# Kernel optimization log

Measured on AMD Instinct MI355X. Metric: run time of the kernel, lower is better.

## Reference

```python
import jax, jax.numpy as jnp
import numpy as np
import math

EPS = 1e-7
N, M, K, D_IN, D_OUT = 8192, 32, 8, 64, 64
KP_EXTENT = 0.66

# ---- Lorentz manifold (curvature k = 1) helpers ----

def l_inner(x, y):
    # Lorentzian inner product, keepdim on last axis
    return -x[..., :1] * y[..., :1] + jnp.sum(x[..., 1:] * y[..., 1:], axis=-1, keepdims=True)

def l_dist(x, y):
    alpha = jnp.clip(-l_inner(x, y), 1.0 + EPS, None)
    return jnp.arccosh(alpha)[..., 0]

def expmap0(u):
    # u: tangent at origin, time component ignored-by-construction (zero)
    sp = u[..., 1:]
    un = jnp.sqrt(jnp.clip(jnp.sum(sp * sp, axis=-1, keepdims=True), 1e-14, None))
    return jnp.concatenate([jnp.cosh(un), jnp.sinh(un) * sp / un], axis=-1)

def expmap(x, u):
    un = jnp.sqrt(jnp.clip(l_inner(u, u), 1e-14, None))
    return jnp.cosh(un) * x + jnp.sinh(un) * u / un

def logmap(x, y):
    alpha = jnp.clip(-l_inner(x, y), 1.0 + EPS, None)
    d = jnp.arccosh(alpha)
    nom = y - alpha * x
    den = jnp.sqrt(jnp.clip(alpha * alpha - 1.0, 1e-14, None))
    return d * nom / den

def ptransp(x, y, v):
    # parallel transport of v from x to y
    return v + l_inner(y, v) / (1.0 - l_inner(x, y)) * (x + y)

def norm_midpoint(ave):
    den = jnp.sqrt(jnp.clip(jnp.abs(l_inner(ave, ave)), 1e-8, None))
    return ave / den


def setup_inputs() -> dict:
    key = jax.random.key(0)
    k1, k2, k3, k4, k5, k6 = jax.random.split(key, 6)
    # points on the hyperboloid: time = sqrt(1 + ||space||^2)
    sp = jax.random.normal(k1, (N, D_IN - 1), dtype=jnp.float32) * 0.5
    t = jnp.sqrt(1.0 + jnp.sum(sp * sp, axis=-1, keepdims=True))
    x = jnp.concatenate([t, sp], axis=-1)
    nei = jax.random.randint(k2, (N, M), 0, N, dtype=jnp.int32)
    nei_mask = jax.random.randint(k3, (N, M), 0, 2, dtype=jnp.int32)
    # kernel points: tangent vectors at origin (time comp 0), first point = center
    kp_sp = jax.random.normal(k4, (K, D_IN - 1), dtype=jnp.float32)
    kp_sp = kp_sp / jnp.linalg.norm(kp_sp, axis=-1, keepdims=True)
    radii = jax.random.uniform(k5, (K, 1), dtype=jnp.float32) * KP_EXTENT
    kp_sp = kp_sp * radii
    kp_sp = kp_sp.at[0].set(0.0)
    kernel_points = jnp.concatenate([jnp.zeros((K, 1), jnp.float32), kp_sp], axis=-1)
    # K LorentzLinear params
    stdv = 1.0 / math.sqrt(D_OUT)
    W = jax.random.uniform(k6, (K, D_OUT, D_IN), dtype=jnp.float32, minval=-stdv, maxval=stdv)
    W = W.at[:, :, 0].set(0.0)  # reset_parameters zeros first input column
    b = jnp.zeros((K, D_OUT), dtype=jnp.float32)
    scale = jnp.full((K,), math.log(10.0), dtype=jnp.float32)
    return {"x": x, "nei": nei, "nei_mask": nei_mask, "W": W, "b": b,
            "scale": scale, "kernel_points": kernel_points}


def reference(x, nei, nei_mask, W, b, scale, kernel_points):
    n, d = x.shape
    x_nei = x[nei]                      # [n, m, d] gather
    xr = x[:, None, :]                  # [n, 1, d]
    og_row = jnp.zeros((d,), x.dtype).at[0].set(1.0)
    # transport_x: map each neighborhood to the origin's tangent frame
    v = logmap(xr, x_nei)
    x0_nei = expmap0(ptransp(xr, og_row[None, None, :], v))   # [n, m, d]
    # kernel positions at the origin (transp=True => base point is origin)
    tmp = expmap(og_row[None, :], ptransp(og_row[None, :], og_row[None, :], kernel_points[1:]))
    x_kernel = jnp.concatenate([tmp, og_row[None, :]], axis=0)  # [K, d]
    # geodesic distances neighbor <-> kernel point: [n, K, m]
    dis = l_dist(x0_nei[:, None, :, :], x_kernel[None, :, None, :])
    dis = dis * nei_mask[:, None, :].astype(x.dtype)
    # K LorentzLinear transforms (vectorized over K): [n, K, m, d_out]
    h = jnp.einsum('nmd,kod->nkmo', x0_nei, W) + b[None, :, None, :]
    time = jax.nn.sigmoid(h[..., :1]) * jnp.exp(scale)[None, :, None, None] + 1.0001
    nar = h[..., 1:]
    s = (time * time - 1.0) / jnp.clip(jnp.sum(nar * nar, axis=-1, keepdims=True), 1e-8, None)
    xt = jnp.concatenate([time, nar * jnp.sqrt(s)], axis=-1)
    # weighted Lorentz midpoint over kernel points, per neighbor: [n, m, d_out]
    per_nei = norm_midpoint(jnp.einsum('nkm,nkmo->nmo', dis, xt))
    # unweighted Lorentz midpoint over neighbors: [n, d_out]
    return norm_midpoint(per_nei.mean(axis=1))
```

## Files before the change

### kernel.cpp

```cpp
#include <hip/hip_runtime.h>
#include <hip/hip_bf16.h>

#define N_NODES 8192
#define M_NEI   32
#define K_PTS   8
#define D       64
#define EPS_    1e-7f

typedef float f4v __attribute__((ext_vector_type(4)));
typedef short s8v __attribute__((ext_vector_type(8)));

__device__ __forceinline__ ushort f2bf(float f) {
  __hip_bfloat16 h = __float2bfloat16(f);
  return *reinterpret_cast<ushort*>(&h);
}
__device__ __forceinline__ float bf2f(ushort u) {
  __hip_bfloat16 h;
  *reinterpret_cast<ushort*>(&h) = u;
  return __bfloat162float(h);
}
__device__ __forceinline__ float frcp(float x)  { return __builtin_amdgcn_rcpf(x); }
__device__ __forceinline__ float frsq(float x)  { return __builtin_amdgcn_rsqf(x); }
__device__ __forceinline__ float fsqrt(float x) { return __builtin_amdgcn_sqrtf(x); }
__device__ __forceinline__ float facosh(float a) {
  float den = fsqrt(fmaxf(a * a - 1.f, 1e-14f));
  return __logf(a + den);
}

template<int CTRL>
__device__ __forceinline__ float dppadd(float v) {
  int t = __builtin_amdgcn_update_dpp(0, __float_as_int(v), CTRL, 0xf, 0xf, true);
  return v + __int_as_float(t);
}
template<int CTRL>
__device__ __forceinline__ float dppmov(float v) {
  return __int_as_float(__builtin_amdgcn_update_dpp(0, __float_as_int(v), CTRL, 0xf, 0xf, true));
}
__device__ __forceinline__ float swz_xor4(float v) {
  return __int_as_float(__builtin_amdgcn_ds_swizzle(__float_as_int(v), 0x101F));
}
__device__ __forceinline__ float sum8(float v) {
  v = dppadd<0xB1>(v);
  v = dppadd<0x4E>(v);
  v = dppadd<0x141>(v);
  return v;
}
__device__ __forceinline__ float sum16(float v) {
  v = dppadd<0x121>(v);
  v = dppadd<0x122>(v);
  v = dppadd<0x124>(v);
  v = dppadd<0x128>(v);
  return v;
}

__global__ void prep_xk(const float* __restrict__ kp, const float* __restrict__ scale,
                        float* __restrict__ xk) {
  int d = threadIdx.x;
  for (int kk = 0; kk < K_PTS - 1; ++kk) {
    float v = kp[(kk + 1) * D + d];
    float p = (d == 0) ? 0.f : v * v;
    #pragma unroll
    for (int s = 1; s < 64; s <<= 1) p += __shfl_xor(p, s);
    float un = sqrtf(fmaxf(p, 1e-14f));
    float sh = sinhf(un) / un;
    xk[kk * D + d] = (d == 0) ? coshf(un) : sh * v;
  }
  xk[(K_PTS - 1) * D + d] = (d == 0) ? 1.f : 0.f;
  if (d < K_PTS) xk[K_PTS * D + d] = expf(scale[d]);
}

__global__ void prep_wb(const float* __restrict__ W, ushort* __restrict__ WF) {
  int idx = blockIdx.x * 256 + threadIdx.x;
  int k    = idx >> 9;
  int ct   = (idx >> 7) & 3;
  int ks   = (idx >> 6) & 1;
  int lane = idx & 63;
  int o  = ct * 16 + (lane & 15);
  int db = (lane >> 4) * 8 + ks * 32;
  const float* wrow = W + (k * 64 + o) * 64 + db;
  s8v hi, lo;
  #pragma unroll
  for (int j = 0; j < 8; ++j) {
    float w = wrow[j];
    ushort h = f2bf(w);
    hi[j] = (short)h;
    lo[j] = (short)f2bf(w - bf2f(h));
  }
  int f = (k * 4 + ct) * 2 + ks;
  *(s8v*)(WF + (size_t)(f * 2 + 0) * 512 + lane * 8) = hi;
  *(s8v*)(WF + (size_t)(f * 2 + 1) * 512 + lane * 8) = lo;
}

__launch_bounds__(256, 4)
__global__ void kpa_main(const float* __restrict__ x, const int* __restrict__ nei,
                         const int* __restrict__ mask, const ushort* __restrict__ WF,
                         const float* __restrict__ b, const float* __restrict__ scale,
                         const float* __restrict__ xk, float* __restrict__ out) {
  __shared__ __align__(16) float  xr_s[D];
  __shared__ __align__(16) float  xk_s[K_PTS * D];
  __shared__ __align__(16) ushort Ah_lds[M_NEI * D];
  __shared__ __align__(16) ushort Al_lds[M_NEI * D];
  __shared__ float dis_s[K_PTS * 33];
  __shared__ __align__(8)  float  hss[K_PTS * M_NEI * 2];
  __shared__ __align__(16) float  red_h[2][16 * 68];
  __shared__ __align__(16) float  redp2[2][64];

  const int n  = blockIdx.x;
  const int t  = threadIdx.x;
  const int w4 = t >> 6;
  const int l  = t & 63;
  const int cl = l & 15;
  const int gr = l >> 4;
  const int wm = w4 & 1;
  const int wk = w4 >> 1;

  if (t < D) xr_s[t] = x[n * D + t];
  xk_s[t] = xk[t]; xk_s[t + 256] = xk[t + 256];
  __syncthreads();

  {
    const int m  = t >> 3;
    const int l8 = t & 7;
    const int d0 = l8 * 8;
    const int ni = nei[n * M_NEI + m];
    float y[8], xr[8];
    float y0 = x[ni * D];
    {
      float4 ya = *(const float4*)(x + ni * D + d0);
      float4 yb = *(const float4*)(x + ni * D + d0 + 4);
      y[0]=ya.x; y[1]=ya.y; y[2]=ya.z; y[3]=ya.w;
      y[4]=yb.x; y[5]=yb.y; y[6]=yb.z; y[7]=yb.w;
      float4 ra = *(const float4*)(xr_s + d0);
      float4 rb = *(const float4*)(xr_s + d0 + 4);
      xr[0]=ra.x; xr[1]=ra.y; xr[2]=ra.z; xr[3]=ra.w;
      xr[4]=rb.x; xr[5]=rb.y; xr[6]=rb.z; xr[7]=rb.w;
    }
    const float xr0 = xr_s[0];
    float p = 0.f;
    #pragma unroll
    for (int j = 0; j < 8; ++j) p += xr[j] * y[j];
    if (l8 == 0) p -= 2.f * xr[0] * y[0];
    p = sum8(p);
    float alpha = fmaxf(-p, 1.f + EPS_);
    float den = fsqrt(fmaxf(alpha * alpha - 1.f, 1e-14f));
    float dd  = __logf(alpha + den);
    float f   = dd * frcp(den);
    float v[8];
    #pragma unroll
    for (int j = 0; j < 8; ++j) v[j] = f * (y[j] - alpha * xr[j]);
    float v0 = f * (y0 - alpha * xr0);
    float c  = -v0 * frcp(1.f + xr0);
    float wv[8];
    float q = 0.f;
    #pragma unroll
    for (int j = 0; j < 8; ++j) { wv[j] = v[j] + c * xr[j]; q += wv[j] * wv[j]; }
    if (l8 == 0) q -= wv[0] * wv[0];
    q = sum8(q);
    float un = fsqrt(fmaxf(q, 1e-14f));
    float e  = __expf(un);
    float ei = frcp(e);
    float sh = (0.5f * (e - ei)) * frcp(un);
    float x0v[8];
    #pragma unroll
    for (int j = 0; j < 8; ++j) x0v[j] = sh * wv[j];
    if (l8 == 0) x0v[0] = 0.5f * (e + ei);
    {
      s8v hi, lo;
      #pragma unroll
      for (int j = 0; j < 8; ++j) {
        uint u = __float_as_uint(x0v[j]);
        hi[j] = (short)(ushort)(u >> 16);
        float lof = x0v[j] - __uint_as_float(u & 0xffff0000u);
        uint ul = __float_as_uint(lof);
        lo[j] = (short)(ushort)((ul + 0x7fffu + ((ul >> 16) & 1u)) >> 16);
      }
      int byte = m * 128 + d0 * 2;
      int swz  = byte ^ ((m & 7) << 4);
      *(s8v*)((char*)Ah_lds + swz) = hi;
      *(s8v*)((char*)Al_lds + swz) = lo;
    }
    float msk = (float)mask[n * M_NEI + m];
    if (l8 == 0) x0v[0] = -x0v[0];
    float pk[8];
    #pragma unroll
    for (int kk = 0; kk < K_PTS; ++kk) {
      const float* xkp = xk_s + kk * D + d0;
      float pp = 0.f;
      #pragma unroll
      for (int j = 0; j < 8; ++j) pp += x0v[j] * xkp[j];
      pk[kk] = pp;
    }
    const bool hi4 = (l8 & 4);
    float s1[4];
    #pragma unroll
    for (int j = 0; j < 4; ++j) {
      float give = hi4 ? pk[j] : pk[j + 4];
      float keep = hi4 ? pk[j + 4] : pk[j];
      s1[j] = keep + swz_xor4(give);
    }
    const bool hi2 = (l8 & 2);
    float s2[2];
    #pragma unroll
    for (int j = 0; j < 2; ++j) {
      float give = hi2 ? s1[j] : s1[j + 2];
      float keep = hi2 ? s1[j + 2] : s1[j];
      s2[j] = keep + dppmov<0x4E>(give);
    }
    const bool hi1 = (l8 & 1);
    float give = hi1 ? s2[0] : s2[1];
    float keep = hi1 ? s2[1] : s2[0];
    float mypp = keep + dppmov<0xB1>(give);
    float al_ = fmaxf(-mypp, 1.f + EPS_);
    dis_s[l8 * 33 + m] = facosh(al_) * msk;
  }
  __syncthreads();

  const int row = wm * 16 + cl;
  s8v ah[2], alo[2];
  #pragma unroll
  for (int ks = 0; ks < 2; ++ks) {
    int byte = row * 128 + (gr * 8 + ks * 32) * 2;
    int swz  = byte ^ ((row & 7) << 4);
    ah[ks]  = *(const s8v*)((const char*)Ah_lds + swz);
    alo[ks] = *(const s8v*)((const char*)Al_lds + swz);
  }

  f4v acc[4][4];
  #pragma unroll
  for (int kq = 0; kq < 4; ++kq) {
    const int k = wk * 4 + kq;
    #pragma unroll
    for (int ct = 0; ct < 4; ++ct) {
      float bv = b[k * 64 + ct * 16 + cl];
      f4v a = (f4v){bv, bv, bv, bv};
      #pragma unroll
      for (int ks = 0; ks < 2; ++ks) {
        int fi = (k * 4 + ct) * 2 + ks;
        s8v bh = *(const s8v*)(WF + (size_t)(fi * 2 + 0) * 512 + l * 8);
        s8v bl = *(const s8v*)(WF + (size_t)(fi * 2 + 1) * 512 + l * 8);
        a = __builtin_amdgcn_mfma_f32_16x16x32_bf16(ah[ks],  bh, a, 0, 0, 0);
        a = __builtin_amdgcn_mfma_f32_16x16x32_bf16(ah[ks],  bl, a, 0, 0, 0);
        a = __builtin_amdgcn_mfma_f32_16x16x32_bf16(alo[ks], bh, a, 0, 0, 0);
      }
      acc[kq][ct] = a;
    }
    #pragma unroll
    for (int r = 0; r < 4; ++r) {
      float ss = acc[kq][0][r]*acc[kq][0][r] + acc[kq][1][r]*acc[kq][1][r]
               + acc[kq][2][r]*acc[kq][2][r] + acc[kq][3][r]*acc[kq][3][r];
      ss = sum16(ss);
      if (cl == 0) {
        const int m = wm * 16 + gr * 4 + r;
        float2* hp = (float2*)&hss[(k * M_NEI + m) * 2];
        *hp = make_float2(acc[kq][0][r], ss);
      }
    }
  }
  __syncthreads();

  {
    const int k = t >> 5;
    const int m = t & 31;
    float2 hp = *(const float2*)&hss[(k * M_NEI + m) * 2];
    float h0 = hp.x, ss = hp.y;
    float nar2 = fmaxf(ss - h0 * h0, 1e-8f);
    float es   = xk[K_PTS * D + k];
    float time = es * frcp(1.f + __expf(-h0)) + 1.0001f;
    float sq   = fsqrt(time * time - 1.f) * frsq(nar2);
    float dm   = dis_s[k * 33 + m];
    *(float2*)&hss[(k * M_NEI + m) * 2] = make_float2(dm * sq, dm * time);
  }
  __syncthreads();

  float yacc[4][4];
  #pragma unroll
  for (int r = 0; r < 4; ++r)
    #pragma unroll
    for (int ct = 0; ct < 4; ++ct) yacc[r][ct] = 0.f;

  #pragma unroll
  for (int kq = 0; kq < 4; ++kq) {
    const int k = wk * 4 + kq;
    #pragma unroll
    for (int r = 0; r < 4; ++r) {
      const int m = wm * 16 + gr * 4 + r;
      float2 dd = *(const float2*)&hss[(k * M_NEI + m) * 2];
      yacc[r][0] += (cl == 0) ? dd.y : dd.x * acc[kq][0][r];
      yacc[r][1] += dd.x * acc[kq][1][r];
      yacc[r][2] += dd.x * acc[kq][2][r];
      yacc[r][3] += dd.x * acc[kq][3][r];
    }
  }

  if (wk == 1) {
    #pragma unroll
    for (int r = 0; r < 4; ++r) {
      const int ml = gr * 4 + r;
      float* rw = &red_h[wm][ml * 68];
      rw[cl]      = yacc[r][0];
      rw[16 + cl] = yacc[r][1];
      rw[32 + cl] = yacc[r][2];
      rw[48 + cl] = yacc[r][3];
    }
  }
  __syncthreads();

  if (wk == 0) {
    float s[4] = {0.f, 0.f, 0.f, 0.f};
    #pragma unroll
    for (int r = 0; r < 4; ++r) {
      const int ml = gr * 4 + r;
      const float* rw = &red_h[wm][ml * 68];
      float v0_ = yacc[r][0] + rw[cl];
      float v1_ = yacc[r][1] + rw[16 + cl];
      float v2_ = yacc[r][2] + rw[32 + cl];
      float v3_ = yacc[r][3] + rw[48 + cl];
      float ip = v0_*v0_ + v1_*v1_ + v2_*v2_ + v3_*v3_;
      if (cl == 0) ip -= 2.f * v0_ * v0_;
      ip = sum16(ip);
      float rin = frsq(fmaxf(fabsf(ip), 1e-8f));
      s[0] += v0_ * rin; s[1] += v1_ * rin;
      s[2] += v2_ * rin; s[3] += v3_ * rin;
    }
    #pragma unroll
    for (int j = 0; j < 4; ++j) {
      float z = s[j];
      z += __shfl_xor(z, 16); z += __shfl_xor(z, 32);
      s[j] = z;
    }
    if (gr == 0) {
      #pragma unroll
      for (int j = 0; j < 4; ++j) redp2[wm][j * 16 + cl] = s[j];
    }
  }
  __syncthreads();

  if (t < 16) {
    float mv[4]; float ip = 0.f;
    #pragma unroll
    for (int j = 0; j < 4; ++j) {
      mv[j] = (redp2[0][j * 16 + t] + redp2[1][j * 16 + t]) * (1.f / 32.f);
      ip += mv[j] * mv[j];
    }
    if (t == 0) ip -= 2.f * mv[0] * mv[0];
    ip = sum16(ip);
    float rin = frsq(fmaxf(fabsf(ip), 1e-8f));
    #pragma unroll
    for (int j = 0; j < 4; ++j) out[n * D + j * 16 + t] = mv[j] * rin;
  }
}

extern "C" void kernel_launch(void* const* d_in, const int* in_sizes, int n_in,
                              void* d_out, int out_size, void* d_ws, size_t ws_size,
                              hipStream_t stream) {
  const float* x     = (const float*)d_in[0];
  const int*   nei   = (const int*)d_in[1];
  const int*   mask  = (const int*)d_in[2];
  const float* W     = (const float*)d_in[3];
  const float* b     = (const float*)d_in[4];
  const float* scale = (const float*)d_in[5];
  const float* kp    = (const float*)d_in[6];
  float* out = (float*)d_out;

  ushort* WF = (ushort*)d_ws;
  float*  xk = (float*)(WF + 65536);

  prep_wb<<<16, 256, 0, stream>>>(W, WF);
  prep_xk<<<1, 64, 0, stream>>>(kp, scale, xk);
  kpa_main<<<N_NODES, 256, 0, stream>>>(x, nei, mask, WF, b, scale, xk, out);
}
```

Baseline: 103.2 us.

## Remove block barriers by wave-local hss handoff and split final reduction across waves

The per-block x row is now read straight from global memory instead of being staged in LDS, which removes the first barrier. The h-to-weight stage is remapped so each wave processes only the hss entries it wrote, which removes two __syncthreads. The cross-wave reduction is split so all four waves each normalise half the rows, and the final midpoint runs on 64 lanes instead of 16. The goal is to cut barrier stalls and idle waves in a short, latency-bound kernel. Correctness now depends on LDS ordering within a wave, with no block barrier between the hss write and read.

```diff
diff --git a/kernel.cpp b/kernel.cpp
--- a/kernel.cpp
+++ b/kernel.cpp
@@ -96,14 +96,13 @@
                          const int* __restrict__ mask, const ushort* __restrict__ WF,
                          const float* __restrict__ b, const float* __restrict__ scale,
                          const float* __restrict__ xk, float* __restrict__ out) {
-  __shared__ __align__(16) float  xr_s[D];
-  __shared__ __align__(16) float  xk_s[K_PTS * D];
+  __shared__ __align__(16) float  xk_s[K_PTS * D + 8];
   __shared__ __align__(16) ushort Ah_lds[M_NEI * D];
   __shared__ __align__(16) ushort Al_lds[M_NEI * D];
   __shared__ float dis_s[K_PTS * 33];
   __shared__ __align__(8)  float  hss[K_PTS * M_NEI * 2];
-  __shared__ __align__(16) float  red_h[2][16 * 68];
-  __shared__ __align__(16) float  redp2[2][64];
+  __shared__ __align__(16) float  red_e[2][2][8 * 68];
+  __shared__ __align__(16) float  redp3[4][64];
 
   const int n  = blockIdx.x;
   const int t  = threadIdx.x;
@@ -114,15 +113,15 @@
   const int wm = w4 & 1;
   const int wk = w4 >> 1;
 
-  if (t < D) xr_s[t] = x[n * D + t];
   xk_s[t] = xk[t]; xk_s[t + 256] = xk[t + 256];
-  __syncthreads();
-
+  if (t < 8) xk_s[512 + t] = xk[512 + t];
+
+  const int mP  = t >> 3;
+  const int l8  = t & 7;
+  float x0v[8];
   {
-    const int m  = t >> 3;
-    const int l8 = t & 7;
     const int d0 = l8 * 8;
-    const int ni = nei[n * M_NEI + m];
+    const int ni = nei[n * M_NEI + mP];
     float y[8], xr[8];
     float y0 = x[ni * D];
     {
@@ -130,12 +129,12 @@
       float4 yb = *(const float4*)(x + ni * D + d0 + 4);
       y[0]=ya.x; y[1]=ya.y; y[2]=ya.z; y[3]=ya.w;
       y[4]=yb.x; y[5]=yb.y; y[6]=yb.z; y[7]=yb.w;
-      float4 ra = *(const float4*)(xr_s + d0);
-      float4 rb = *(const float4*)(xr_s + d0 + 4);
+      float4 ra = *(const float4*)(x + n * D + d0);
+      float4 rb = *(const float4*)(x + n * D + d0 + 4);
       xr[0]=ra.x; xr[1]=ra.y; xr[2]=ra.z; xr[3]=ra.w;
       xr[4]=rb.x; xr[5]=rb.y; xr[6]=rb.z; xr[7]=rb.w;
     }
-    const float xr0 = xr_s[0];
+    const float xr0 = x[n * D];
     float p = 0.f;
     #pragma unroll
     for (int j = 0; j < 8; ++j) p += xr[j] * y[j];
@@ -160,7 +159,6 @@
     float e  = __expf(un);
     float ei = frcp(e);
     float sh = (0.5f * (e - ei)) * frcp(un);
-    float x0v[8];
     #pragma unroll
     for (int j = 0; j < 8; ++j) x0v[j] = sh * wv[j];
     if (l8 == 0) x0v[0] = 0.5f * (e + ei);
@@ -174,12 +172,17 @@
         uint ul = __float_as_uint(lof);
         lo[j] = (short)(ushort)((ul + 0x7fffu + ((ul >> 16) & 1u)) >> 16);
       }
-      int byte = m * 128 + d0 * 2;
-      int swz  = byte ^ ((m & 7) << 4);
+      int byte = mP * 128 + d0 * 2;
+      int swz  = byte ^ ((mP & 7) << 4);
       *(s8v*)((char*)Ah_lds + swz) = hi;
       *(s8v*)((char*)Al_lds + swz) = lo;
     }
-    float msk = (float)mask[n * M_NEI + m];
+  }
+  __syncthreads();
+
+  {
+    const int d0 = l8 * 8;
+    float msk = (float)mask[n * M_NEI + mP];
     if (l8 == 0) x0v[0] = -x0v[0];
     float pk[8];
     #pragma unroll
@@ -211,7 +214,7 @@
     float keep = hi1 ? s2[1] : s2[0];
     float mypp = keep + dppmov<0xB1>(give);
     float al_ = fmaxf(-mypp, 1.f + EPS_);
-    dis_s[l8 * 33 + m] = facosh(al_) * msk;
+    dis_s[l8 * 33 + mP] = facosh(al_) * msk;
   }
   __syncthreads();
 
@@ -251,26 +254,23 @@
       ss = sum16(ss);
       if (cl == 0) {
         const int m = wm * 16 + gr * 4 + r;
-        float2* hp = (float2*)&hss[(k * M_NEI + m) * 2];
-        *hp = make_float2(acc[kq][0][r], ss);
+        *(float2*)&hss[(k * M_NEI + m) * 2] = make_float2(acc[kq][0][r], ss);
       }
     }
   }
-  __syncthreads();
 
   {
-    const int k = t >> 5;
-    const int m = t & 31;
-    float2 hp = *(const float2*)&hss[(k * M_NEI + m) * 2];
+    const int kB = wk * 4 + (l >> 4);
+    const int mB = wm * 16 + (l & 15);
+    float2 hp = *(const float2*)&hss[(kB * M_NEI + mB) * 2];
     float h0 = hp.x, ss = hp.y;
     float nar2 = fmaxf(ss - h0 * h0, 1e-8f);
-    float es   = xk[K_PTS * D + k];
+    float es   = xk_s[512 + kB];
     float time = es * frcp(1.f + __expf(-h0)) + 1.0001f;
     float sq   = fsqrt(time * time - 1.f) * frsq(nar2);
-    float dm   = dis_s[k * 33 + m];
-    *(float2*)&hss[(k * M_NEI + m) * 2] = make_float2(dm * sq, dm * time);
-  }
-  __syncthreads();
+    float dm   = dis_s[kB * 33 + mB];
+    *(float2*)&hss[(kB * M_NEI + mB) * 2] = make_float2(dm * sq, dm * time);
+  }
 
   float yacc[4][4];
   #pragma unroll
@@ -292,25 +292,23 @@
     }
   }
 
-  if (wk == 1) {
-    #pragma unroll
-    for (int r = 0; r < 4; ++r) {
-      const int ml = gr * 4 + r;
-      float* rw = &red_h[wm][ml * 68];
-      rw[cl]      = yacc[r][0];
-      rw[16 + cl] = yacc[r][1];
-      rw[32 + cl] = yacc[r][2];
-      rw[48 + cl] = yacc[r][3];
-    }
+  #pragma unroll
+  for (int j = 0; j < 2; ++j) {
+    const int rp = (1 - wk) * 2 + j;
+    float* rw = &red_e[1 - wk][wm][(gr * 2 + j) * 68];
+    rw[cl]      = yacc[rp][0];
+    rw[16 + cl] = yacc[rp][1];
+    rw[32 + cl] = yacc[rp][2];
+    rw[48 + cl] = yacc[rp][3];
   }
   __syncthreads();
 
-  if (wk == 0) {
+  {
     float s[4] = {0.f, 0.f, 0.f, 0.f};
     #pragma unroll
-    for (int r = 0; r < 4; ++r) {
-      const int ml = gr * 4 + r;
-      const float* rw = &red_h[wm][ml * 68];
+    for (int j = 0; j < 2; ++j) {
+      const int r = wk * 2 + j;
+      const float* rw = &red_e[wk][wm][(gr * 2 + j) * 68];
       float v0_ = yacc[r][0] + rw[cl];
       float v1_ = yacc[r][1] + rw[16 + cl];
       float v2_ = yacc[r][2] + rw[32 + cl];
@@ -323,30 +321,24 @@
       s[2] += v2_ * rin; s[3] += v3_ * rin;
     }
     #pragma unroll
-    for (int j = 0; j < 4; ++j) {
-      float z = s[j];
+    for (int j2 = 0; j2 < 4; ++j2) {
+      float z = s[j2];
       z += __shfl_xor(z, 16); z += __shfl_xor(z, 32);
-      s[j] = z;
+      s[j2] = z;
     }
     if (gr == 0) {
       #pragma unroll
-      for (int j = 0; j < 4; ++j) redp2[wm][j * 16 + cl] = s[j];
+      for (int j2 = 0; j2 < 4; ++j2) redp3[w4][j2 * 16 + cl] = s[j2];
     }
   }
   __syncthreads();
 
-  if (t < 16) {
-    float mv[4]; float ip = 0.f;
-    #pragma unroll
-    for (int j = 0; j < 4; ++j) {
-      mv[j] = (redp2[0][j * 16 + t] + redp2[1][j * 16 + t]) * (1.f / 32.f);
-      ip += mv[j] * mv[j];
-    }
-    if (t == 0) ip -= 2.f * mv[0] * mv[0];
+  if (t < 64) {
+    float mv = (redp3[0][t] + redp3[1][t] + redp3[2][t] + redp3[3][t]) * (1.f / 32.f);
+    float ip = (t == 0) ? -mv * mv : mv * mv;
     ip = sum16(ip);
-    float rin = frsq(fmaxf(fabsf(ip), 1e-8f));
-    #pragma unroll
-    for (int j = 0; j < 4; ++j) out[n * D + j * 16 + t] = mv[j] * rin;
+    ip += __shfl_xor(ip, 16); ip += __shfl_xor(ip, 32);
+    out[n * D + t] = mv * frsq(fmaxf(fabsf(ip), 1e-8f));
   }
 }
 
```

New measurement: 151.1 us. 1.46x slower.
